# Performance work log

Hardware: AMD Instinct MI355X
Metric: run time of the kernel (lower is better)

Reference implementation:

```python
import jax, jax.numpy as jnp
import numpy as np

DIM = 1024
HEADS = 16
HEAD_DIM = DIM // HEADS
FF_MULT = 2
ROPE_BASE = 10000.0
EPS = 1e-6
B, S = 2, 2048


def setup_inputs() -> dict:
    key = jax.random.key(0)
    ks = jax.random.split(key, 6)
    sc = lambda fan_in: 1.0 / np.sqrt(fan_in)
    return {
        "x": jax.random.normal(ks[0], (B, S, DIM), dtype=jnp.float32),
        "w_in_norm": jnp.ones((DIM,), dtype=jnp.float32),
        "w_ff_norm": jnp.ones((DIM,), dtype=jnp.float32),
        "w_qkv": jax.random.normal(ks[1], (3 * DIM, DIM), dtype=jnp.float32) * sc(DIM),
        "w_out": jax.random.normal(ks[2], (DIM, DIM), dtype=jnp.float32) * sc(DIM),
        "w_fc": jax.random.normal(ks[3], (DIM * FF_MULT, DIM), dtype=jnp.float32) * sc(DIM),
        "w_proj": jax.random.normal(ks[4], (DIM, DIM * FF_MULT), dtype=jnp.float32) * sc(DIM * FF_MULT),
    }


def rmsnorm(x, w):
    var = jnp.mean(jnp.square(x), axis=-1, keepdims=True)
    return x * jax.lax.rsqrt(var + EPS) * w


def rope_tables(seq_len):
    half = HEAD_DIM // 2
    inv_freq = 1.0 / (ROPE_BASE ** (2.0 * jnp.arange(half, dtype=jnp.float32) / HEAD_DIM))
    angles = jnp.arange(seq_len, dtype=jnp.float32)[:, None] * inv_freq[None, :]  # (S, half)
    return jnp.cos(angles), jnp.sin(angles)


def apply_rope(x, cos, sin):
    # x: (B, H, S, D); interleaved pairs along last dim
    xp = x.reshape(*x.shape[:-1], HEAD_DIM // 2, 2)
    x_even, x_odd = xp[..., 0], xp[..., 1]
    c = cos.astype(x.dtype)  # (S, half) broadcasts over (B, H)
    s = sin.astype(x.dtype)
    rot_even = x_even * c - x_odd * s
    rot_odd = x_odd * c + x_even * s
    return jnp.stack([rot_even, rot_odd], axis=-1).reshape(x.shape)


def reference(x, w_in_norm, w_ff_norm, w_qkv, w_out, w_fc, w_proj):
    b, s, d = x.shape
    # --- attention sub-block (pre-norm) ---
    h = rmsnorm(x, w_in_norm)
    qkv = jnp.einsum("bsd,ed->bse", h, w_qkv)  # (B, S, 3*D)
    q, k, v = jnp.split(qkv, 3, axis=-1)
    def heads(t):
        return t.reshape(b, s, HEADS, HEAD_DIM).transpose(0, 2, 1, 3)  # (B, H, S, Dh)
    q, k, v = heads(q), heads(k), heads(v)
    cos, sin = rope_tables(s)
    q = apply_rope(q, cos, sin)
    k = apply_rope(k, cos, sin)
    scale = 1.0 / np.sqrt(HEAD_DIM)
    scores = jnp.einsum("bhqd,bhkd->bhqk", q, k) * scale
    causal = jnp.tril(jnp.ones((s, s), dtype=bool))
    scores = jnp.where(causal, scores, jnp.finfo(scores.dtype).min)
    probs = jax.nn.softmax(scores, axis=-1)
    attn = jnp.einsum("bhqk,bhkd->bhqd", probs, v)
    attn = attn.transpose(0, 2, 1, 3).reshape(b, s, d)
    x = x + jnp.einsum("bsd,ed->bse", attn, w_out)
    # --- feed-forward sub-block (pre-norm) ---
    h = rmsnorm(x, w_ff_norm)
    hid = jax.nn.silu(jnp.einsum("bsd,fd->bsf", h, w_fc))
    x = x + jnp.einsum("bsf,df->bsd", hid, w_proj)
    return x
```

## Files before the change

### kernel.cpp

```cpp
#include <hip/hip_runtime.h>
#include <hip/hip_bf16.h>
#include <cstdint>

#define DIMSZ 1024
#define S_LEN 2048
#define NH 16
#define HD 64

typedef __attribute__((ext_vector_type(4))) float f32x4;
typedef __attribute__((ext_vector_type(8))) __bf16 bf16x8;

#define MFMA_BF16(a,b,c) __builtin_amdgcn_mfma_f32_16x16x32_bf16((a),(b),(c),0,0,0)

__device__ __forceinline__ void gload_lds16(const void* g, void* l) {
  __builtin_amdgcn_global_load_lds(
      (const __attribute__((address_space(1))) unsigned int*)(uintptr_t)g,
      (__attribute__((address_space(3))) unsigned int*)(uintptr_t)l,
      16, 0, 0);
}

__device__ __forceinline__ float bf16bits2f(unsigned short u) {
  return __uint_as_float((unsigned)u << 16);
}

__global__ __launch_bounds__(256)
void prep_kernel(const float* __restrict__ s0, const float* __restrict__ s1,
                 const float* __restrict__ s2, const float* __restrict__ s3,
                 __hip_bfloat16* __restrict__ d0, __hip_bfloat16* __restrict__ d1,
                 __hip_bfloat16* __restrict__ d2, __hip_bfloat16* __restrict__ d3,
                 const float* __restrict__ x, const float* __restrict__ w_in,
                 __hip_bfloat16* __restrict__ h)
{
  __shared__ float red[4];
  const int bid = blockIdx.x;
  const int tid = threadIdx.x;
  if (bid < 8192) {
    int i = bid * 256 + tid;
    const float* s; __hip_bfloat16* d; int off;
    if (i < 786432)       { s = s0; d = d0; off = i; }
    else if (i < 1048576) { s = s1; d = d1; off = i - 786432; }
    else if (i < 1572864) { s = s2; d = d2; off = i - 1048576; }
    else                  { s = s3; d = d3; off = i - 1572864; }
    float4 v = ((const float4*)s)[off];
    __hip_bfloat16* o = d + (size_t)off * 4;
    o[0] = __float2bfloat16(v.x);
    o[1] = __float2bfloat16(v.y);
    o[2] = __float2bfloat16(v.z);
    o[3] = __float2bfloat16(v.w);
    return;
  }
  const int row = bid - 8192;
  const float4 v = ((const float4*)(x + (size_t)row * DIMSZ))[tid];
  float ss = v.x*v.x + v.y*v.y + v.z*v.z + v.w*v.w;
  #pragma unroll
  for (int m = 32; m >= 1; m >>= 1) ss += __shfl_xor(ss, m);
  int wave = tid >> 6, lane = tid & 63;
  if (lane == 0) red[wave] = ss;
  __syncthreads();
  float tot = red[0] + red[1] + red[2] + red[3];
  float sc = rsqrtf(tot * (1.0f / DIMSZ) + 1e-6f);
  const float4 wv = ((const float4*)w_in)[tid];
  __hip_bfloat16* o = h + (size_t)row * DIMSZ + tid * 4;
  o[0] = __float2bfloat16(v.x * sc * wv.x);
  o[1] = __float2bfloat16(v.y * sc * wv.y);
  o[2] = __float2bfloat16(v.z * sc * wv.z);
  o[3] = __float2bfloat16(v.w * sc * wv.w);
}

__global__ __launch_bounds__(256)
void rmsnorm_bf16_kernel(const __hip_bfloat16* __restrict__ x, const float* __restrict__ w,
                         __hip_bfloat16* __restrict__ out)
{
  int row = blockIdx.x;
  int tid = threadIdx.x;
  const ushort4 raw = ((const ushort4*)(x + (size_t)row * DIMSZ))[tid];
  float v0 = bf16bits2f(raw.x), v1 = bf16bits2f(raw.y);
  float v2 = bf16bits2f(raw.z), v3 = bf16bits2f(raw.w);
  float ss = v0*v0 + v1*v1 + v2*v2 + v3*v3;
  #pragma unroll
  for (int m = 32; m >= 1; m >>= 1) ss += __shfl_xor(ss, m);
  __shared__ float red[4];
  int wave = tid >> 6, lane = tid & 63;
  if (lane == 0) red[wave] = ss;
  __syncthreads();
  float tot = red[0] + red[1] + red[2] + red[3];
  float sc = rsqrtf(tot * (1.0f / DIMSZ) + 1e-6f);
  const float4 wv = ((const float4*)w)[tid];
  __hip_bfloat16* o = out + (size_t)row * DIMSZ + tid * 4;
  o[0] = __float2bfloat16(v0 * sc * wv.x);
  o[1] = __float2bfloat16(v1 * sc * wv.y);
  o[2] = __float2bfloat16(v2 * sc * wv.z);
  o[3] = __float2bfloat16(v3 * sc * wv.w);
}

template<int EPI>
__global__ __launch_bounds__(256, 2)
void gemm_bt2(const __hip_bfloat16* __restrict__ A,
              const __hip_bfloat16* __restrict__ Bw,
              float* __restrict__ Cf,
              __hip_bfloat16* __restrict__ Cb,
              const float* __restrict__ residf,
              const __hip_bfloat16* __restrict__ residb,
              int N, int K)
{
  __shared__ __align__(16) char sA[2][16384];
  __shared__ __align__(16) char sB[2][16384];
  const int tid = threadIdx.x;
  const int wave = tid >> 6, lane = tid & 63;
  const int lg = lane >> 4, lr15 = lane & 15;
  const int row0 = blockIdx.y * 128, col0 = blockIdx.x * 128;
  const int wr = wave >> 1, wc = wave & 1;
  f32x4 acc[4][4] = {};

  const size_t Kb = (size_t)K * 2;
  const int rown = tid >> 3;
  const int scol = ((tid & 7) << 4) ^ ((rown & 7) << 4);
  const char* gA = (const char*)A + (size_t)(row0 + rown) * Kb + scol;
  const char* gB = (const char*)Bw + (size_t)(col0 + rown) * Kb + scol;
  const int dbase = wave * 1024;

  const int nsteps = K >> 6;
  int cur = 0;

#define STAGE_G(buf, st) do {                                              \
    const size_t kb_ = (size_t)(st) * 128;                                 \
    _Pragma("unroll")                                                      \
    for (int it = 0; it < 4; ++it) {                                       \
      gload_lds16(gA + (size_t)(it * 32) * Kb + kb_, &sA[buf][it * 4096 + dbase]); \
      gload_lds16(gB + (size_t)(it * 32) * Kb + kb_, &sB[buf][it * 4096 + dbase]); \
    }                                                                      \
  } while (0)

  STAGE_G(0, 0);
  __syncthreads();

  const int swz = (lr15 & 7) << 4;
  for (int st = 0; st < nsteps; ++st) {
    if (st + 1 < nsteps) STAGE_G(cur ^ 1, st + 1);
    const char* pA = sA[cur];
    const char* pB = sB[cur];
    bf16x8 af[2][4], bfr[2][4];
    #pragma unroll
    for (int m = 0; m < 4; ++m) {
      const int ra = (wr * 64 + m * 16 + lr15) * 128;
      af[0][m] = *(const bf16x8*)(pA + ra + ((lg * 16) ^ swz));
      af[1][m] = *(const bf16x8*)(pA + ra + ((64 + lg * 16) ^ swz));
      const int rb = (wc * 64 + m * 16 + lr15) * 128;
      bfr[0][m] = *(const bf16x8*)(pB + rb + ((lg * 16) ^ swz));
      bfr[1][m] = *(const bf16x8*)(pB + rb + ((64 + lg * 16) ^ swz));
    }
    #pragma unroll
    for (int kh = 0; kh < 2; ++kh)
      #pragma unroll
      for (int m = 0; m < 4; ++m)
        #pragma unroll
        for (int n = 0; n < 4; ++n)
          acc[m][n] = MFMA_BF16(af[kh][m], bfr[kh][n], acc[m][n]);
    __syncthreads();
    cur ^= 1;
  }
#undef STAGE_G

  #pragma unroll
  for (int m = 0; m < 4; ++m) {
    #pragma unroll
    for (int n = 0; n < 4; ++n) {
      #pragma unroll
      for (int r = 0; r < 4; ++r) {
        const int grow = row0 + wr * 64 + m * 16 + lg * 4 + r;
        const int gcol = col0 + wc * 64 + n * 16 + lr15;
        const size_t idx = (size_t)grow * N + gcol;
        const float v = acc[m][n][r];
        if (EPI == 0) {
          Cb[idx] = __float2bfloat16(v);
        } else if (EPI == 1) {
          Cb[idx] = __float2bfloat16(residf[idx] + v);
        } else if (EPI == 2) {
          Cb[idx] = __float2bfloat16(v / (1.0f + __expf(-v)));
        } else {
          Cf[idx] = __bfloat162float(residb[idx]) + v;
        }
      }
    }
  }
}

__global__ __launch_bounds__(256)
void rope_vt_kernel(const __hip_bfloat16* __restrict__ qkv,
                    __hip_bfloat16* __restrict__ Q, __hip_bfloat16* __restrict__ Kx,
                    __hip_bfloat16* __restrict__ Vt)
{
  __shared__ __hip_bfloat16 t[64][72];
  const int bid = blockIdx.x;
  const int tid = threadIdx.x;
  if (bid < 8192) {
    int idx = bid * 256 + tid;
    int i = idx & 31;
    int h = (idx >> 5) & 15;
    int s = (idx >> 9) & (S_LEN - 1);
    int b = idx >> 20;
    const size_t base = ((size_t)b * S_LEN + s) * 3072 + h * 64 + 2 * i;
    float qe = __bfloat162float(qkv[base]);
    float qo = __bfloat162float(qkv[base + 1]);
    float ke = __bfloat162float(qkv[base + 1024]);
    float ko = __bfloat162float(qkv[base + 1025]);
    float inv = __expf(-(2.0f * i) * (9.210340371976184f / 64.0f));
    float ang = (float)s * inv;
    float sn, cs;
    __sincosf(ang, &sn, &cs);
    const float sc = 0.125f;
    size_t qb = (((size_t)b * NH + h) * S_LEN + s) * HD + 2 * i;
    Q[qb]     = __float2bfloat16((qe * cs - qo * sn) * sc);
    Q[qb + 1] = __float2bfloat16((qo * cs + qe * sn) * sc);
    Kx[qb]     = __float2bfloat16(ke * cs - ko * sn);
    Kx[qb + 1] = __float2bfloat16(ko * cs + ke * sn);
    return;
  }
  const int v = bid - 8192;
  const int bh = v >> 5;
  const int s0 = (v & 31) * 64;
  const int b = bh >> 4, h = bh & 15;
  const int c = tid & 63;
  #pragma unroll
  for (int r = 0; r < 16; ++r) {
    int srow = r * 4 + (tid >> 6);
    t[srow][c] = qkv[((size_t)b * S_LEN + s0 + srow) * 3072 + 2048 + h * 64 + c];
  }
  __syncthreads();
  #pragma unroll
  for (int r = 0; r < 16; ++r) {
    int drow = r * 4 + (tid >> 6);
    Vt[(((size_t)b * NH + h) * HD + drow) * S_LEN + s0 + c] = t[c][drow];
  }
}

__device__ __forceinline__ unsigned bf16pack2(float a, float b) {
  __hip_bfloat16 ha = __float2bfloat16(a), hb = __float2bfloat16(b);
  unsigned ua = *reinterpret_cast<unsigned short*>(&ha);
  unsigned ub = *reinterpret_cast<unsigned short*>(&hb);
  return ua | (ub << 16);
}

__global__ __launch_bounds__(512, 4)
void flash_attn4(const __hip_bfloat16* __restrict__ Q,
                 const __hip_bfloat16* __restrict__ Kx,
                 const __hip_bfloat16* __restrict__ Vt,
                 __hip_bfloat16* __restrict__ attn)
{
  __shared__ __align__(16) char sK[2][8192];
  __shared__ __align__(16) char sV[2][8192];
  __shared__ __align__(16) char sP[8][2048];

  const int tid = threadIdx.x;
  const int w = tid >> 6;
  const int lane = tid & 63;
  const int lg = lane >> 4, lr = lane & 15;
  const int bid = blockIdx.x;
  const int bh = bid & 31;
  const int b = bh >> 4, h = bh & 15;
  const int u = (bid >> 5) & 7;
  const int rnd = bid >> 8;
  const int qb = rnd == 0 ? (u << 1) : (15 - (u << 1));
  const int q0 = qb << 7;
  const int nsteps = (qb << 1) + 2;

  const char* Kb = (const char*)(Kx + (size_t)bh * S_LEN * HD);
  const char* Vb = (const char*)(Vt + (size_t)bh * HD * S_LEN);
  const __hip_bfloat16* Qp = Q + (size_t)bh * S_LEN * HD;

  const int q0w = q0 + w * 16;
  const bf16x8 qf0 = *(const bf16x8*)&Qp[(q0w + lr) * HD + lg * 8];
  const bf16x8 qf1 = *(const bf16x8*)&Qp[(q0w + lr) * HD + 32 + lg * 8];
  char* sPw = sP[w];
  const int swzr = (lr & 7) << 4;
  const int srow = tid >> 3;
  const int scol = ((tid & 7) << 4) ^ ((srow & 7) << 4);
  const int wbase = w << 10;

  f32x4 acc[4] = {};
  float lsum = 0.f;
  int cur = 0;

  gload_lds16(Kb + (size_t)srow * 128 + scol, sK[0] + wbase);
  gload_lds16(Vb + (size_t)srow * (S_LEN * 2) + scol, sV[0] + wbase);
  __syncthreads();

  for (int st = 0; st < nsteps; ++st) {
    if (st + 1 < nsteps) {
      const size_t kn = (size_t)(st + 1) * 64;
      gload_lds16(Kb + (kn + srow) * 128 + scol, sK[cur ^ 1] + wbase);
      gload_lds16(Vb + (size_t)srow * (S_LEN * 2) + kn * 2 + scol, sV[cur ^ 1] + wbase);
    }
    const int k0 = st * 64;
    const char* pK = sK[cur];
    const char* pV = sV[cur];
    f32x4 sv[4];
    __builtin_amdgcn_s_setprio(1);
    #pragma unroll
    for (int t = 0; t < 4; ++t) {
      const int rb = (t * 16 + lr) * 128;
      const bf16x8 kf0 = *(const bf16x8*)(pK + rb + ((lg * 16) ^ swzr));
      const bf16x8 kf1 = *(const bf16x8*)(pK + rb + ((64 + lg * 16) ^ swzr));
      f32x4 z = {};
      z = MFMA_BF16(kf0, qf0, z);
      z = MFMA_BF16(kf1, qf1, z);
      sv[t] = z;
    }
    __builtin_amdgcn_s_setprio(0);
    const bool maskstep = (st >= nsteps - 2);
    #pragma unroll
    for (int t = 0; t < 4; ++t) {
      float p[4];
      #pragma unroll
      for (int r = 0; r < 4; ++r) {
        float e = __expf(sv[t][r]);
        if (maskstep) {
          const int kg = k0 + t * 16 + lg * 4 + r;
          e = (kg <= q0w + lr) ? e : 0.f;
        }
        lsum += e;
        p[r] = e;
      }
      uint2 wv2;
      wv2.x = bf16pack2(p[0], p[1]);
      wv2.y = bf16pack2(p[2], p[3]);
      *(uint2*)(sPw + lr * 128 + ((t * 32 + lg * 8) ^ swzr)) = wv2;
    }
    asm volatile("s_waitcnt lgkmcnt(0)" ::: "memory");
    __builtin_amdgcn_sched_barrier(0);
    const bf16x8 pa0 = *(const bf16x8*)(sPw + lr * 128 + ((lg * 16) ^ swzr));
    const bf16x8 pa1 = *(const bf16x8*)(sPw + lr * 128 + ((64 + lg * 16) ^ swzr));
    __builtin_amdgcn_s_setprio(1);
    #pragma unroll
    for (int dt = 0; dt < 4; ++dt) {
      const int rb = (dt * 16 + lr) * 128;
      const bf16x8 vf0 = *(const bf16x8*)(pV + rb + ((lg * 16) ^ swzr));
      const bf16x8 vf1 = *(const bf16x8*)(pV + rb + ((64 + lg * 16) ^ swzr));
      acc[dt] = MFMA_BF16(pa0, vf0, acc[dt]);
      acc[dt] = MFMA_BF16(pa1, vf1, acc[dt]);
    }
    __builtin_amdgcn_s_setprio(0);
    __syncthreads();
    cur ^= 1;
  }

  lsum += __shfl_xor(lsum, 16);
  lsum += __shfl_xor(lsum, 32);
  #pragma unroll
  for (int r = 0; r < 4; ++r) {
    const float li = __shfl(lsum, lg * 4 + r);
    const float rli = 1.0f / li;
    const size_t rowb = ((size_t)b * S_LEN + q0w + lg * 4 + r) * DIMSZ + h * HD;
    #pragma unroll
    for (int dt = 0; dt < 4; ++dt)
      attn[rowb + dt * 16 + lr] = __float2bfloat16(acc[dt][r] * rli);
  }
}

extern "C" void kernel_launch(void* const* d_in, const int* in_sizes, int n_in,
                              void* d_out, int out_size, void* d_ws, size_t ws_size,
                              hipStream_t stream)
{
  const float* x      = (const float*)d_in[0];
  const float* w_in   = (const float*)d_in[1];
  const float* w_ff   = (const float*)d_in[2];
  const float* w_qkv  = (const float*)d_in[3];
  const float* w_out  = (const float*)d_in[4];
  const float* w_fc   = (const float*)d_in[5];
  const float* w_proj = (const float*)d_in[6];
  float* out = (float*)d_out;
  char* ws = (char*)d_ws;

  __hip_bfloat16* wq_b   = (__hip_bfloat16*)(ws);
  __hip_bfloat16* wo_b   = (__hip_bfloat16*)(ws + 6291456);
  __hip_bfloat16* wfc_b  = (__hip_bfloat16*)(ws + 8388608);
  __hip_bfloat16* wpr_b  = (__hip_bfloat16*)(ws + 12582912);
  __hip_bfloat16* h_b    = (__hip_bfloat16*)(ws + 16777216);
  __hip_bfloat16* qkv_b  = (__hip_bfloat16*)(ws + 25165824);
  __hip_bfloat16* attn_b = (__hip_bfloat16*)(ws + 25165824);
  __hip_bfloat16* hid_b  = (__hip_bfloat16*)(ws + 33554432);
  __hip_bfloat16* Q_b    = (__hip_bfloat16*)(ws + 50331648);
  __hip_bfloat16* K_b    = (__hip_bfloat16*)(ws + 58720256);
  __hip_bfloat16* Vt_b   = (__hip_bfloat16*)(ws + 67108864);
  __hip_bfloat16* x1b    = (__hip_bfloat16*)(ws + 50331648);

  prep_kernel<<<8192 + 4096, 256, 0, stream>>>(w_qkv, w_out, w_fc, w_proj,
                                               wq_b, wo_b, wfc_b, wpr_b, x, w_in, h_b);
  gemm_bt2<0><<<dim3(3072 / 128, 4096 / 128), 256, 0, stream>>>(h_b, wq_b, nullptr, qkv_b, nullptr, nullptr, 3072, 1024);
  rope_vt_kernel<<<8192 + 1024, 256, 0, stream>>>(qkv_b, Q_b, K_b, Vt_b);
  flash_attn4<<<512, 512, 0, stream>>>(Q_b, K_b, Vt_b, attn_b);
  gemm_bt2<1><<<dim3(1024 / 128, 4096 / 128), 256, 0, stream>>>(attn_b, wo_b, nullptr, x1b, x, nullptr, 1024, 1024);
  rmsnorm_bf16_kernel<<<4096, 256, 0, stream>>>(x1b, w_ff, h_b);
  gemm_bt2<2><<<dim3(2048 / 128, 4096 / 128), 256, 0, stream>>>(h_b, wfc_b, nullptr, hid_b, nullptr, nullptr, 2048, 1024);
  gemm_bt2<3><<<dim3(1024 / 128, 4096 / 128), 256, 0, stream>>>(hid_b, wpr_b, out, nullptr, nullptr, x1b, 1024, 2048);
}
```

Before: 169.5 us.

## Move remaining weight casts into attention tail; compute softmax sum via MFMA

The fp32-to-bf16 conversion of w_out, w_fc and w_proj is moved out of the prep kernel and into the tail of the attention kernel. There it is done by the blocks with the shorter causal workloads, so the load-imbalanced attention phase absorbs the casts. The softmax row sum is now accumulated with an extra MFMA against a ones vector instead of scalar adds plus shuffles. Packing uses the native v_cvt_pk_bf16_f32 instruction. The risk is that the denominator is now summed from bf16-rounded probabilities, and the attention kernel gains memory traffic and register pressure.

```diff
diff --git a/kernel.cpp b/kernel.cpp
--- a/kernel.cpp
+++ b/kernel.cpp
@@ -23,33 +23,31 @@
   return __uint_as_float((unsigned)u << 16);
 }
 
+__device__ __forceinline__ unsigned cvt_pk_bf16(float lo, float hi) {
+  unsigned r;
+  asm("v_cvt_pk_bf16_f32 %0, %1, %2" : "=v"(r) : "v"(lo), "v"(hi));
+  return r;
+}
+
 __global__ __launch_bounds__(256)
-void prep_kernel(const float* __restrict__ s0, const float* __restrict__ s1,
-                 const float* __restrict__ s2, const float* __restrict__ s3,
-                 __hip_bfloat16* __restrict__ d0, __hip_bfloat16* __restrict__ d1,
-                 __hip_bfloat16* __restrict__ d2, __hip_bfloat16* __restrict__ d3,
+void prep_kernel(const float* __restrict__ wq_f, __hip_bfloat16* __restrict__ wq_b,
                  const float* __restrict__ x, const float* __restrict__ w_in,
                  __hip_bfloat16* __restrict__ h)
 {
   __shared__ float red[4];
   const int bid = blockIdx.x;
   const int tid = threadIdx.x;
-  if (bid < 8192) {
-    int i = bid * 256 + tid;
-    const float* s; __hip_bfloat16* d; int off;
-    if (i < 786432)       { s = s0; d = d0; off = i; }
-    else if (i < 1048576) { s = s1; d = d1; off = i - 786432; }
-    else if (i < 1572864) { s = s2; d = d2; off = i - 1048576; }
-    else                  { s = s3; d = d3; off = i - 1572864; }
-    float4 v = ((const float4*)s)[off];
-    __hip_bfloat16* o = d + (size_t)off * 4;
+  if (bid < 3072) {
+    int off = bid * 256 + tid;
+    float4 v = ((const float4*)wq_f)[off];
+    __hip_bfloat16* o = wq_b + (size_t)off * 4;
     o[0] = __float2bfloat16(v.x);
     o[1] = __float2bfloat16(v.y);
     o[2] = __float2bfloat16(v.z);
     o[3] = __float2bfloat16(v.w);
     return;
   }
-  const int row = bid - 8192;
+  const int row = bid - 3072;
   const float4 v = ((const float4*)(x + (size_t)row * DIMSZ))[tid];
   float ss = v.x*v.x + v.y*v.y + v.z*v.z + v.w*v.w;
   #pragma unroll
@@ -234,18 +232,15 @@
   }
 }
 
-__device__ __forceinline__ unsigned bf16pack2(float a, float b) {
-  __hip_bfloat16 ha = __float2bfloat16(a), hb = __float2bfloat16(b);
-  unsigned ua = *reinterpret_cast<unsigned short*>(&ha);
-  unsigned ub = *reinterpret_cast<unsigned short*>(&hb);
-  return ua | (ub << 16);
-}
-
 __global__ __launch_bounds__(512, 4)
-void flash_attn4(const __hip_bfloat16* __restrict__ Q,
+void flash_attn7(const __hip_bfloat16* __restrict__ Q,
                  const __hip_bfloat16* __restrict__ Kx,
                  const __hip_bfloat16* __restrict__ Vt,
-                 __hip_bfloat16* __restrict__ attn)
+                 __hip_bfloat16* __restrict__ attn,
+                 const float* __restrict__ wo_f, const float* __restrict__ wfc_f,
+                 const float* __restrict__ wpr_f,
+                 __hip_bfloat16* __restrict__ wo_b, __hip_bfloat16* __restrict__ wfc_b,
+                 __hip_bfloat16* __restrict__ wpr_b)
 {
   __shared__ __align__(16) char sK[2][8192];
   __shared__ __align__(16) char sV[2][8192];
@@ -277,8 +272,12 @@
   const int scol = ((tid & 7) << 4) ^ ((srow & 7) << 4);
   const int wbase = w << 10;
 
+  bf16x8 ones;
+  #pragma unroll
+  for (int i = 0; i < 8; ++i) ones[i] = (__bf16)1.0f;
+
   f32x4 acc[4] = {};
-  float lsum = 0.f;
+  f32x4 acc_l = {};
   int cur = 0;
 
   gload_lds16(Kb + (size_t)srow * 128 + scol, sK[0] + wbase);
@@ -318,12 +317,11 @@
           const int kg = k0 + t * 16 + lg * 4 + r;
           e = (kg <= q0w + lr) ? e : 0.f;
         }
-        lsum += e;
         p[r] = e;
       }
       uint2 wv2;
-      wv2.x = bf16pack2(p[0], p[1]);
-      wv2.y = bf16pack2(p[2], p[3]);
+      wv2.x = cvt_pk_bf16(p[0], p[1]);
+      wv2.y = cvt_pk_bf16(p[2], p[3]);
       *(uint2*)(sPw + lr * 128 + ((t * 32 + lg * 8) ^ swzr)) = wv2;
     }
     asm volatile("s_waitcnt lgkmcnt(0)" ::: "memory");
@@ -339,21 +337,39 @@
       acc[dt] = MFMA_BF16(pa0, vf0, acc[dt]);
       acc[dt] = MFMA_BF16(pa1, vf1, acc[dt]);
     }
+    acc_l = MFMA_BF16(pa0, ones, acc_l);
+    acc_l = MFMA_BF16(pa1, ones, acc_l);
     __builtin_amdgcn_s_setprio(0);
     __syncthreads();
     cur ^= 1;
   }
 
-  lsum += __shfl_xor(lsum, 16);
-  lsum += __shfl_xor(lsum, 32);
   #pragma unroll
   for (int r = 0; r < 4; ++r) {
-    const float li = __shfl(lsum, lg * 4 + r);
-    const float rli = 1.0f / li;
+    const float rli = 1.0f / acc_l[r];
     const size_t rowb = ((size_t)b * S_LEN + q0w + lg * 4 + r) * DIMSZ + h * HD;
     #pragma unroll
     for (int dt = 0; dt < 4; ++dt)
       attn[rowb + dt * 16 + lr] = __float2bfloat16(acc[dt][r] * rli);
+  }
+
+  if ((rnd == 0) ? (u < 4) : (u >= 4)) {
+    const int cid = (bh << 3) | u;
+    const int base = cid * 512 + tid;
+    #pragma unroll
+    for (int i = 0; i < 10; ++i) {
+      const int f = i * 131072 + base;
+      const float* s; __hip_bfloat16* d; int off;
+      if (f < 262144)      { s = wo_f;  d = wo_b;  off = f; }
+      else if (f < 786432) { s = wfc_f; d = wfc_b; off = f - 262144; }
+      else                 { s = wpr_f; d = wpr_b; off = f - 786432; }
+      float4 v = ((const float4*)s)[off];
+      __hip_bfloat16* o = d + (size_t)off * 4;
+      o[0] = __float2bfloat16(v.x);
+      o[1] = __float2bfloat16(v.y);
+      o[2] = __float2bfloat16(v.z);
+      o[3] = __float2bfloat16(v.w);
+    }
   }
 }
 
@@ -384,11 +400,11 @@
   __hip_bfloat16* Vt_b   = (__hip_bfloat16*)(ws + 67108864);
   __hip_bfloat16* x1b    = (__hip_bfloat16*)(ws + 50331648);
 
-  prep_kernel<<<8192 + 4096, 256, 0, stream>>>(w_qkv, w_out, w_fc, w_proj,
-                                               wq_b, wo_b, wfc_b, wpr_b, x, w_in, h_b);
+  prep_kernel<<<3072 + 4096, 256, 0, stream>>>(w_qkv, wq_b, x, w_in, h_b);
   gemm_bt2<0><<<dim3(3072 / 128, 4096 / 128), 256, 0, stream>>>(h_b, wq_b, nullptr, qkv_b, nullptr, nullptr, 3072, 1024);
   rope_vt_kernel<<<8192 + 1024, 256, 0, stream>>>(qkv_b, Q_b, K_b, Vt_b);
-  flash_attn4<<<512, 512, 0, stream>>>(Q_b, K_b, Vt_b, attn_b);
+  flash_attn7<<<512, 512, 0, stream>>>(Q_b, K_b, Vt_b, attn_b,
+                                       w_out, w_fc, w_proj, wo_b, wfc_b, wpr_b);
   gemm_bt2<1><<<dim3(1024 / 128, 4096 / 128), 256, 0, stream>>>(attn_b, wo_b, nullptr, x1b, x, nullptr, 1024, 1024);
   rmsnorm_bf16_kernel<<<4096, 256, 0, stream>>>(x1b, w_ff, h_b);
   gemm_bt2<2><<<dim3(2048 / 128, 4096 / 128), 256, 0, stream>>>(h_b, wfc_b, nullptr, hid_b, nullptr, nullptr, 2048, 1024);
```

Result: faster. 162.4 us (-4.2%).
